# Performance work log

Hardware: AMD Instinct MI355X
Metric: run time of the kernel (lower is better)

Reference implementation:

```python
import jax, jax.numpy as jnp
import numpy as np

B, S, HID, NH = 4, 8192, 1024, 32
DH = HID // NH  # 32 == NH, required by the module's broadcast multiply


def setup_inputs() -> dict:
    key = jax.random.key(0)
    ks = jax.random.split(key, 9)
    scale = 1.0 / np.sqrt(HID)
    return {
        "query": jax.random.normal(ks[0], (B, S, HID), jnp.float32),
        "key": jax.random.normal(ks[1], (B, S, HID), jnp.float32),
        "value": jax.random.normal(ks[2], (B, S, HID), jnp.float32),
        "Wq": jax.random.normal(ks[3], (HID, HID), jnp.float32) * scale,
        "bq": jnp.zeros((HID,), jnp.float32),
        "Wk": jax.random.normal(ks[4], (HID, HID), jnp.float32) * scale,
        "bk": jnp.zeros((HID,), jnp.float32),
        "Wv": jax.random.normal(ks[5], (HID, HID), jnp.float32) * scale,
        "bv": jnp.zeros((HID,), jnp.float32),
    }


def reference(query, key, value, Wq, bq, Wk, bk, Wv, bv):
    # Linear projections (torch Linear: x @ W.T + b)
    q = (query @ Wq.T + bq).reshape(B, S, NH, DH)
    k = (key @ Wk.T + bk).reshape(B, S, NH, DH)
    v = (value @ Wv.T + bv).reshape(B, S, NH, DH)
    # NOTE: source does NOT transpose heads to a batch dim, so matmul
    # contracts head_dim per-token: scores[b,s,h,t] over heads h,t.
    scores = jnp.einsum('bshd,bstd->bsht', q, k) / jnp.sqrt(jnp.float32(HID))
    scores = jax.nn.softmax(scores, axis=-1)  # softmax over heads axis t
    # Dropout is identity in inference mode.
    # Elementwise broadcast multiply [B,S,H,H] * [B,S,H,DH] (H == DH)
    out = scores * v
    return out.reshape(B, S, HID)
```

## Files before the change

kernel.cpp:

```cpp
#include <hip/hip_runtime.h>
#include <hip/hip_bf16.h>


typedef __attribute__((ext_vector_type(8))) short bf16x8;
typedef __attribute__((ext_vector_type(4))) float f32x4;

#define HID 1024

#define GLOAD_LDS16(gp, lp)                                                   \
  __builtin_amdgcn_global_load_lds(                                           \
      (const __attribute__((address_space(1))) void*)(gp),                    \
      (__attribute__((address_space(3))) void*)(lp), 16, 0, 0)

#define SBAR __builtin_amdgcn_sched_barrier(0)

__device__ __forceinline__ unsigned short f2bf(float f) {
  unsigned int u = __builtin_bit_cast(unsigned int, f);
  u += 0x7FFFu + ((u >> 16) & 1u);
  return (unsigned short)(u >> 16);
}
__device__ __forceinline__ float bf2f(unsigned short h) {
  unsigned int u = (unsigned int)h << 16;
  return __builtin_bit_cast(float, u);
}

__device__ __forceinline__ uint2 cvt4(f32x4 a) {
  uint2 r;
  asm("v_cvt_pk_bf16_f32 %0, %1, %2" : "=v"(r.x) : "v"(a[0]), "v"(a[1]));
  asm("v_cvt_pk_bf16_f32 %0, %1, %2" : "=v"(r.y) : "v"(a[2]), "v"(a[3]));
  return r;
}
__device__ __forceinline__ bf16x8 cvt8(f32x4 a, f32x4 b) {
  union { unsigned int u[4]; bf16x8 v; } r;
  asm("v_cvt_pk_bf16_f32 %0, %1, %2" : "=v"(r.u[0]) : "v"(a[0]), "v"(a[1]));
  asm("v_cvt_pk_bf16_f32 %0, %1, %2" : "=v"(r.u[1]) : "v"(a[2]), "v"(a[3]));
  asm("v_cvt_pk_bf16_f32 %0, %1, %2" : "=v"(r.u[2]) : "v"(b[0]), "v"(b[1]));
  asm("v_cvt_pk_bf16_f32 %0, %1, %2" : "=v"(r.u[3]) : "v"(b[2]), "v"(b[3]));
  return r.v;
}

__global__ __launch_bounds__(256)
void convw_kernel(const float* __restrict__ src, unsigned short* __restrict__ dst) {
  const int i = blockIdx.x * 256 + threadIdx.x;
  const f32x4 a = ((const f32x4*)src)[i * 2];
  const f32x4 b = ((const f32x4*)src)[i * 2 + 1];
  ((bf16x8*)dst)[i] = cvt8(a, b);
}

template<int MODE>
__global__ __launch_bounds__(512, 1)
void gemm256(const float* __restrict__ X, const unsigned short* __restrict__ Wb,
             const float* __restrict__ bias, void* outp,
             const unsigned short* __restrict__ pbf) {
  const int bid = blockIdx.x;
  const int L = (bid & 7) * 64 + (bid >> 3);
  const int m0 = (L >> 2) * 256;
  const int n0 = (L & 3) * 256;
  const int tid = threadIdx.x;
  const int lane = tid & 63;
  const int wid = tid >> 6;
  const int wm = (wid >> 2) * 128;
  const int wn = (wid & 3) * 64;
  const int lo = lane & 15, grp = lane >> 4;

  __shared__ __align__(16) unsigned char lds[2][65536];

  const char* Xc = (const char*)X;
  const int acg = tid & 15;
  size_t asrc[8]; int aldst[8];
#pragma unroll
  for (int i = 0; i < 8; ++i) {
    const int row = i * 32 + (tid >> 4);
    asrc[i] = (size_t)(m0 + row) * 4096 + (size_t)(acg * 16);
    aldst[i] = row * 128 + (((acg >> 1) ^ (row & 7)) << 4) + (acg & 1) * 8;
  }
  f32x4 ar[8];
  auto aload = [&](int kt) {
    const size_t kb = (size_t)kt * 256;
#pragma unroll
    for (int i = 0; i < 8; ++i) ar[i] = *(const f32x4*)(Xc + asrc[i] + kb);
  };
  auto awrite = [&](int b) {
#pragma unroll
    for (int i = 0; i < 8; ++i) *(uint2*)&lds[b][aldst[i]] = cvt4(ar[i]);
  };

  const char* Wc = (const char*)Wb;
  size_t bsrc[4];
#pragma unroll
  for (int i = 0; i < 4; ++i) {
    const int g = tid + i * 512;
    const int row = g >> 3, j = g & 7;
    bsrc[i] = (size_t)(n0 + row) * 2048 + (size_t)((j ^ (row & 7)) << 4);
  }
  auto bstage = [&](int b, int kt) {
    const size_t kb = (size_t)kt * 128;
#pragma unroll
    for (int i = 0; i < 4; ++i)
      GLOAD_LDS16(Wc + bsrc[i] + kb, &lds[b][32768 + tid * 16 + i * 8192]);
  };

  f32x4 acc[8][4] = {};
  auto compute = [&](int b) {
#pragma unroll
    for (int kk = 0; kk < 2; ++kk) {
      const int s = kk * 4 + grp;
      bf16x8 af[8], bfm[4];
#pragma unroll
      for (int f = 0; f < 8; ++f) {
        const int ra = wm + f * 16 + lo;
        af[f] = *(const bf16x8*)&lds[b][ra * 128 + ((s ^ (ra & 7)) << 4)];
      }
#pragma unroll
      for (int g = 0; g < 4; ++g) {
        const int rb = wn + g * 16 + lo;
        bfm[g] = *(const bf16x8*)&lds[b][32768 + rb * 128 + ((s ^ (rb & 7)) << 4)];
      }
      __builtin_amdgcn_s_setprio(1);
#pragma unroll
      for (int fm = 0; fm < 8; ++fm)
#pragma unroll
        for (int fn = 0; fn < 4; ++fn)
          acc[fm][fn] = __builtin_amdgcn_mfma_f32_16x16x32_bf16(
              af[fm], bfm[fn], acc[fm][fn], 0, 0, 0);
      __builtin_amdgcn_s_setprio(0);
    }
  };

  aload(0);
  awrite(0);
  SBAR;
  bstage(0, 0);
  SBAR;
  aload(1);
  SBAR;
  asm volatile("s_waitcnt vmcnt(8)" ::: "memory");
  asm volatile("s_waitcnt lgkmcnt(0)" ::: "memory");
  __builtin_amdgcn_s_barrier();
  SBAR;

#pragma unroll 1
  for (int kt = 0; kt < 16; ++kt) {
    const int cur = kt & 1;
    if (kt < 15) {
      awrite(cur ^ 1);
      SBAR;
      bstage(cur ^ 1, kt + 1);
      SBAR;
      if (kt < 14) aload(kt + 2);
      SBAR;
    }
    compute(cur);
    SBAR;
    if (kt < 14) asm volatile("s_waitcnt vmcnt(8)" ::: "memory");
    else         asm volatile("s_waitcnt vmcnt(0)" ::: "memory");
    asm volatile("s_waitcnt lgkmcnt(0)" ::: "memory");
    __builtin_amdgcn_s_barrier();
    SBAR;
  }

  if (MODE == 2) {
    float* of = (float*)outp;
#pragma unroll
    for (int fm = 0; fm < 8; ++fm) {
      const int row = m0 + wm + fm * 16 + grp * 4;
#pragma unroll
      for (int fn = 0; fn < 4; ++fn) {
        const int col = n0 + wn + fn * 16 + lo;
        const float bc = bias[col];
#pragma unroll
        for (int j = 0; j < 4; ++j) {
          const size_t idx = (size_t)(row + j) * 1024 + col;
          of[idx] = bf2f(pbf[idx]) * (acc[fm][fn][j] + bc);
        }
      }
    }
  } else {
    const float scale = (MODE == 0) ? 0.03125f : 1.0f;
    unsigned short* lds16 = (unsigned short*)&lds[0][0];
    unsigned short* ob = (unsigned short*)outp;
    const int half = (MODE == 1) ? 1024 : 0;
    float bcol[4];
#pragma unroll
    for (int fn = 0; fn < 4; ++fn) bcol[fn] = bias[n0 + wn + fn * 16 + lo];
#pragma unroll 1
    for (int h = 0; h < 2; ++h) {
      if ((wid >> 2) == h) {
#pragma unroll
        for (int fm = 0; fm < 8; ++fm)
#pragma unroll
          for (int fn = 0; fn < 4; ++fn)
#pragma unroll
            for (int j = 0; j < 4; ++j) {
              const int rl = fm * 16 + grp * 4 + j;
              const int col = wn + fn * 16 + lo;
              lds16[rl * 256 + (col ^ (grp << 4))] =
                  f2bf((acc[fm][fn][j] + bcol[fn]) * scale);
            }
      }
      __syncthreads();
      {
        const int row = tid >> 2;
        const int c0 = (tid & 3) * 64;
        const int x = ((row >> 2) & 3) << 4;
#pragma unroll
        for (int q = 0; q < 8; ++q) {
          const int cg = c0 + q * 8;
          const uint4 v = *(const uint4*)&lds16[row * 256 + (cg ^ x)];
          *(uint4*)&ob[(size_t)(m0 + h * 128 + row) * 2048 + half + n0 + cg] = v;
        }
      }
      __syncthreads();
    }
  }
}

template<int MODE>
__global__ __launch_bounds__(256, 2)
void gemm_fb(const float* __restrict__ X, const float* __restrict__ W,
             const float* __restrict__ bias, void* outp,
             const unsigned short* __restrict__ pbf, int use_ws) {
  const int bid = blockIdx.x;
  const int L = (bid & 7) * 256 + (bid >> 3);
  const int m0 = (L >> 3) * 128;
  const int n0 = (L & 7) * 128;
  const int tid = threadIdx.x;
  const int lane = tid & 63;
  const int wid = tid >> 6;
  const int wm = (wid >> 1) << 6;
  const int wn = (wid & 1) << 6;
  const int lo = lane & 15, grp = lane >> 4;
  __shared__ __align__(16) unsigned char lds[2][32768];
  const int srow = tid >> 3;
  const int sk8  = tid & 7;
  const float* Ag = X + (size_t)(m0 + srow) * HID + sk8 * 8;
  const float* Bg = W + (size_t)(n0 + srow) * HID + sk8 * 8;
  f32x4 la[4][2], lb[4][2];
  auto gload = [&](int k0) {
#pragma unroll
    for (int rr = 0; rr < 4; ++rr) {
      const float* ap = Ag + (size_t)(rr * 32) * HID + k0;
      const float* bp = Bg + (size_t)(rr * 32) * HID + k0;
      la[rr][0] = *(const f32x4*)(ap); la[rr][1] = *(const f32x4*)(ap + 4);
      lb[rr][0] = *(const f32x4*)(bp); lb[rr][1] = *(const f32x4*)(bp + 4);
    }
  };
  auto cvtwrite = [&](int b) {
#pragma unroll
    for (int rr = 0; rr < 4; ++rr) {
      const int row = srow + rr * 32;
      const int adr = row * 128 + ((sk8 ^ (row & 7)) << 4);
      *(bf16x8*)&lds[b][adr]         = cvt8(la[rr][0], la[rr][1]);
      *(bf16x8*)&lds[b][16384 + adr] = cvt8(lb[rr][0], lb[rr][1]);
    }
  };
  f32x4 acc[4][4] = {};
  auto compute = [&](int b) {
#pragma unroll
    for (int kk = 0; kk < 2; ++kk) {
      const int slot = kk * 4 + grp;
      bf16x8 af[4], bfm[4];
#pragma unroll
      for (int f = 0; f < 4; ++f) {
        const int ra = wm + f * 16 + lo;
        const int rb = wn + f * 16 + lo;
        af[f]  = *(const bf16x8*)&lds[b][ra * 128 + ((slot ^ (ra & 7)) << 4)];
        bfm[f] = *(const bf16x8*)&lds[b][16384 + rb * 128 + ((slot ^ (rb & 7)) << 4)];
      }
#pragma unroll
      for (int fm = 0; fm < 4; ++fm)
#pragma unroll
        for (int fn = 0; fn < 4; ++fn)
          acc[fm][fn] = __builtin_amdgcn_mfma_f32_16x16x32_bf16(
              af[fm], bfm[fn], acc[fm][fn], 0, 0, 0);
    }
  };
  gload(0); cvtwrite(0); gload(64);
  SBAR;
  asm volatile("s_waitcnt lgkmcnt(0)" ::: "memory");
  __builtin_amdgcn_s_barrier();
  SBAR;
#pragma unroll 1
  for (int kt = 0; kt < 16; ++kt) {
    compute(kt & 1);
    if (kt < 15) {
      cvtwrite((kt + 1) & 1);
      if (kt < 14) gload((kt + 2) * 64);
    }
    SBAR;
    asm volatile("s_waitcnt lgkmcnt(0)" ::: "memory");
    __builtin_amdgcn_s_barrier();
    SBAR;
  }
  unsigned char* eb = &lds[0][0];
  const unsigned char* ebc = eb;
  if (MODE == 2) {
    float* of = (float*)outp;
#pragma unroll
    for (int fm = 0; fm < 4; ++fm) {
      const int row = m0 + wm + fm * 16 + grp * 4;
#pragma unroll
      for (int fn = 0; fn < 4; ++fn) {
        const int col = n0 + wn + fn * 16 + lo;
        const float bc = bias[col];
#pragma unroll
        for (int j = 0; j < 4; ++j) {
          const size_t idx = (size_t)(row + j) * 1024 + col;
          const float p = use_ws ? bf2f(pbf[idx]) : of[idx];
          of[idx] = p * (acc[fm][fn][j] + bc);
        }
      }
    }
  } else {
    const float scale = (MODE == 0) ? 0.03125f : 1.0f;
#pragma unroll
    for (int fm = 0; fm < 4; ++fm) {
#pragma unroll
      for (int fn = 0; fn < 4; ++fn) {
        const int colL = wn + fn * 16 + lo;
        const float bc = bias[n0 + colL];
#pragma unroll
        for (int j = 0; j < 4; ++j) {
          const int rowL = wm + fm * 16 + grp * 4 + j;
          const int byte = rowL * 256 + ((colL * 2) ^ ((rowL & 7) << 5));
          *(unsigned short*)&eb[byte] = f2bf((acc[fm][fn][j] + bc) * scale);
        }
      }
    }
    __syncthreads();
    unsigned short* ob = (unsigned short*)outp;
    const int half = (MODE == 1) ? 1024 : 0;
#pragma unroll
    for (int p = 0; p < 8; ++p) {
      const int r = p * 16 + (tid >> 4);
      const int c0 = (tid & 15) * 8;
      const uint4 v = *(const uint4*)&ebc[r * 256 + ((c0 * 2) ^ ((r & 7) << 5))];
      *(uint4*)&ob[(size_t)(m0 + r) * 2048 + half + n0 + c0] = v;
    }
  }
}

template<int PMODE>
__global__ __launch_bounds__(256)
void attn_kernel(float* __restrict__ dout, unsigned short* __restrict__ wsp) {
  const int wid = threadIdx.x >> 6;
  const int lane = threadIdx.x & 63;
  const int token = blockIdx.x * 4 + wid;
  const int lo = lane & 15, grp = lane >> 4;
  const unsigned short* qk = (const unsigned short*)dout + (size_t)token * 2048;
  const int base = lo * 32 + grp * 8;

  bf16x8 a0 = *(const bf16x8*)(qk + base);
  bf16x8 a1 = *(const bf16x8*)(qk + 512 + base);
  bf16x8 b0 = *(const bf16x8*)(qk + 1024 + base);
  bf16x8 b1 = *(const bf16x8*)(qk + 1536 + base);
  asm volatile("s_waitcnt vmcnt(0)" ::: "memory");

  const f32x4 z = {0.f, 0.f, 0.f, 0.f};
  f32x4 s[2][2];
  s[0][0] = __builtin_amdgcn_mfma_f32_16x16x32_bf16(a0, b0, z, 0, 0, 0);
  s[0][1] = __builtin_amdgcn_mfma_f32_16x16x32_bf16(a0, b1, z, 0, 0, 0);
  s[1][0] = __builtin_amdgcn_mfma_f32_16x16x32_bf16(a1, b0, z, 0, 0, 0);
  s[1][1] = __builtin_amdgcn_mfma_f32_16x16x32_bf16(a1, b1, z, 0, 0, 0);

  float* od = dout + (size_t)token * 1024;
  unsigned short* ob = wsp + (size_t)token * 1024;
#pragma unroll
  for (int rt = 0; rt < 2; ++rt) {
#pragma unroll
    for (int j = 0; j < 4; ++j) {
      const float v0 = s[rt][0][j], v1 = s[rt][1][j];
      float m = fmaxf(v0, v1);
#pragma unroll
      for (int msk = 1; msk < 16; msk <<= 1) m = fmaxf(m, __shfl_xor(m, msk, 64));
      const float e0 = __expf(v0 - m), e1 = __expf(v1 - m);
      float ssum = e0 + e1;
#pragma unroll
      for (int msk = 1; msk < 16; msk <<= 1) ssum += __shfl_xor(ssum, msk, 64);
      const float inv = 1.0f / ssum;
      const int h = rt * 16 + grp * 4 + j;
      if (PMODE == 0) {
        od[h * 32 + lo]      = e0 * inv;
        od[h * 32 + 16 + lo] = e1 * inv;
      } else {
        ob[h * 32 + lo]      = f2bf(e0 * inv);
        ob[h * 32 + 16 + lo] = f2bf(e1 * inv);
      }
    }
  }
}

extern "C" void kernel_launch(void* const* d_in, const int* in_sizes, int n_in,
                              void* d_out, int out_size, void* d_ws, size_t ws_size,
                              hipStream_t stream) {
  const float* query = (const float*)d_in[0];
  const float* key   = (const float*)d_in[1];
  const float* value = (const float*)d_in[2];
  const float* Wq    = (const float*)d_in[3];
  const float* bq    = (const float*)d_in[4];
  const float* Wk    = (const float*)d_in[5];
  const float* bk    = (const float*)d_in[6];
  const float* Wv    = (const float*)d_in[7];
  const float* bv    = (const float*)d_in[8];

  const size_t P_BYTES = (size_t)32768 * 1024 * 2;
  const size_t W_BYTES = (size_t)1024 * 1024 * 2;
  unsigned short* pbf = (unsigned short*)d_ws;
  unsigned short* Wqb = (unsigned short*)((char*)d_ws + P_BYTES);
  unsigned short* Wkb = Wqb + (W_BYTES / 2);
  unsigned short* Wvb = Wkb + (W_BYTES / 2);

  if (ws_size >= P_BYTES + 3 * W_BYTES) {
    convw_kernel<<<dim3(512), dim3(256), 0, stream>>>(Wq, Wqb);
    convw_kernel<<<dim3(512), dim3(256), 0, stream>>>(Wk, Wkb);
    convw_kernel<<<dim3(512), dim3(256), 0, stream>>>(Wv, Wvb);
    gemm256<0><<<dim3(512), dim3(512), 0, stream>>>(query, Wqb, bq, d_out, pbf);
    gemm256<1><<<dim3(512), dim3(512), 0, stream>>>(key,   Wkb, bk, d_out, pbf);
    attn_kernel<1><<<dim3(8192), dim3(256), 0, stream>>>((float*)d_out, pbf);
    gemm256<2><<<dim3(512), dim3(512), 0, stream>>>(value, Wvb, bv, d_out, pbf);
  } else {
    const int use_ws = (ws_size >= P_BYTES) ? 1 : 0;
    gemm_fb<0><<<dim3(2048), dim3(256), 0, stream>>>(query, Wq, bq, d_out, nullptr, 0);
    gemm_fb<1><<<dim3(2048), dim3(256), 0, stream>>>(key,   Wk, bk, d_out, nullptr, 0);
    if (use_ws)
      attn_kernel<1><<<dim3(8192), dim3(256), 0, stream>>>((float*)d_out, pbf);
    else
      attn_kernel<0><<<dim3(8192), dim3(256), 0, stream>>>((float*)d_out, nullptr);
    gemm_fb<2><<<dim3(2048), dim3(256), 0, stream>>>(value, Wv, bv, d_out, pbf, use_ws);
  }
}
```

Before: 378.1 us.

## Interleave LDS reads, global prefetch and MFMA in four barrier-synced phases

The GEMM main loop changes from a monolithic stage-then-compute body to four phases per k-tile. Each phase loads part of the A/B fragments from LDS, issues part of the next tile's global-to-LDS staging, then runs a quarter of the MFMAs between workgroup barriers. The goal is to overlap memory traffic with matrix-core work, in the style of ping-pong scheduling, and to cut register pressure by holding only half the A fragments at once. In exchange the loop has more barriers and waits per iteration.

Measured after the change: 412.0 us. 9.0% more time.

```diff
diff --git a/kernel.cpp b/kernel.cpp
--- a/kernel.cpp
+++ b/kernel.cpp
@@ -93,44 +93,57 @@
     const int row = g >> 3, j = g & 7;
     bsrc[i] = (size_t)(n0 + row) * 2048 + (size_t)((j ^ (row & 7)) << 4);
   }
-  auto bstage = [&](int b, int kt) {
+  auto bstage_h = [&](int b, int kt, int h) {
     const size_t kb = (size_t)kt * 128;
 #pragma unroll
-    for (int i = 0; i < 4; ++i)
+    for (int i = 2 * h; i < 2 * h + 2; ++i)
       GLOAD_LDS16(Wc + bsrc[i] + kb, &lds[b][32768 + tid * 16 + i * 8192]);
   };
 
   f32x4 acc[8][4] = {};
-  auto compute = [&](int b) {
-#pragma unroll
-    for (int kk = 0; kk < 2; ++kk) {
-      const int s = kk * 4 + grp;
-      bf16x8 af[8], bfm[4];
-#pragma unroll
-      for (int f = 0; f < 8; ++f) {
-        const int ra = wm + f * 16 + lo;
-        af[f] = *(const bf16x8*)&lds[b][ra * 128 + ((s ^ (ra & 7)) << 4)];
-      }
-#pragma unroll
-      for (int g = 0; g < 4; ++g) {
-        const int rb = wn + g * 16 + lo;
-        bfm[g] = *(const bf16x8*)&lds[b][32768 + rb * 128 + ((s ^ (rb & 7)) << 4)];
-      }
-      __builtin_amdgcn_s_setprio(1);
-#pragma unroll
-      for (int fm = 0; fm < 8; ++fm)
-#pragma unroll
-        for (int fn = 0; fn < 4; ++fn)
-          acc[fm][fn] = __builtin_amdgcn_mfma_f32_16x16x32_bf16(
-              af[fm], bfm[fn], acc[fm][fn], 0, 0, 0);
-      __builtin_amdgcn_s_setprio(0);
-    }
-  };
+  bf16x8 af[4], bfr[4];
+  auto rdB = [&](int b, int kk) {
+#pragma unroll
+    for (int g = 0; g < 4; ++g) {
+      const int rb = wn + g * 16 + lo;
+      bfr[g] = *(const bf16x8*)&lds[b][32768 + rb * 128 +
+                                       (((kk * 4 + grp) ^ (rb & 7)) << 4)];
+    }
+  };
+  auto rdA = [&](int b, int kk, int fh) {
+#pragma unroll
+    for (int f = 0; f < 4; ++f) {
+      const int ra = wm + (fh * 4 + f) * 16 + lo;
+      af[f] = *(const bf16x8*)&lds[b][ra * 128 +
+                                      (((kk * 4 + grp) ^ (ra & 7)) << 4)];
+    }
+  };
+  auto mfma4 = [&](int fh) {
+    __builtin_amdgcn_s_setprio(1);
+#pragma unroll
+    for (int f = 0; f < 4; ++f)
+#pragma unroll
+      for (int g = 0; g < 4; ++g)
+        acc[fh * 4 + f][g] = __builtin_amdgcn_mfma_f32_16x16x32_bf16(
+            af[f], bfr[g], acc[fh * 4 + f][g], 0, 0, 0);
+    __builtin_amdgcn_s_setprio(0);
+  };
+
+#define PHASE_SYNC                                                 \
+  SBAR;                                                            \
+  __builtin_amdgcn_s_barrier();                                    \
+  asm volatile("s_waitcnt lgkmcnt(0)" ::: "memory");               \
+  SBAR;
+#define PHASE_END                                                  \
+  SBAR;                                                            \
+  __builtin_amdgcn_s_barrier();                                    \
+  SBAR;
 
   aload(0);
   awrite(0);
   SBAR;
-  bstage(0, 0);
+  bstage_h(0, 0, 0);
+  bstage_h(0, 0, 1);
   SBAR;
   aload(1);
   SBAR;
@@ -141,20 +154,31 @@
 
 #pragma unroll 1
   for (int kt = 0; kt < 16; ++kt) {
-    const int cur = kt & 1;
-    if (kt < 15) {
-      awrite(cur ^ 1);
-      SBAR;
-      bstage(cur ^ 1, kt + 1);
-      SBAR;
-      if (kt < 14) aload(kt + 2);
-      SBAR;
-    }
-    compute(cur);
+    const int cur = kt & 1, nxt = cur ^ 1;
+    rdB(cur, 0);
+    rdA(cur, 0, 0);
+    if (kt < 15) bstage_h(nxt, kt + 1, 0);
+    PHASE_SYNC;
+    mfma4(0);
+    PHASE_END;
+    rdA(cur, 0, 1);
+    if (kt < 15) bstage_h(nxt, kt + 1, 1);
+    PHASE_SYNC;
+    mfma4(1);
+    PHASE_END;
+    rdB(cur, 1);
+    rdA(cur, 1, 0);
+    if (kt < 15) awrite(nxt);
+    PHASE_SYNC;
+    mfma4(0);
+    PHASE_END;
+    rdA(cur, 1, 1);
+    if (kt < 14) aload(kt + 2);
+    PHASE_SYNC;
+    mfma4(1);
     SBAR;
     if (kt < 14) asm volatile("s_waitcnt vmcnt(8)" ::: "memory");
     else         asm volatile("s_waitcnt vmcnt(0)" ::: "memory");
-    asm volatile("s_waitcnt lgkmcnt(0)" ::: "memory");
     __builtin_amdgcn_s_barrier();
     SBAR;
   }
```

## Deepen GEMM pipeline: triple-buffer B tiles and double A register prefetch

Applied to the files above, without the earlier changes.

Restructures the GEMM main loop so the weight (B) tiles are triple-buffered in LDS and staged two k-steps ahead, while the activation (A) tiles use two register sets loaded three k-steps ahead. The aim is to hide more global-memory latency behind the MFMA compute. In exchange it uses more LDS (160KB per block), more VGPRs for the second register set, and more complex vmcnt accounting that could be fragile.

Result: slower. 780.5 us (+106.4%).

```diff
diff --git a/kernel.cpp b/kernel.cpp
--- a/kernel.cpp
+++ b/kernel.cpp
@@ -63,7 +63,7 @@
   const int wn = (wid & 3) * 64;
   const int lo = lane & 15, grp = lane >> 4;
 
-  __shared__ __align__(16) unsigned char lds[2][65536];
+  __shared__ __align__(16) unsigned char lds[163840];
 
   const char* Xc = (const char*)X;
   const int acg = tid & 15;
@@ -74,15 +74,24 @@
     asrc[i] = (size_t)(m0 + row) * 4096 + (size_t)(acg * 16);
     aldst[i] = row * 128 + (((acg >> 1) ^ (row & 7)) << 4) + (acg & 1) * 8;
   }
-  f32x4 ar[8];
-  auto aload = [&](int kt) {
+  f32x4 ar0[8], ar1[8];
+  auto aload0 = [&](int kt) {
     const size_t kb = (size_t)kt * 256;
 #pragma unroll
-    for (int i = 0; i < 8; ++i) ar[i] = *(const f32x4*)(Xc + asrc[i] + kb);
-  };
-  auto awrite = [&](int b) {
-#pragma unroll
-    for (int i = 0; i < 8; ++i) *(uint2*)&lds[b][aldst[i]] = cvt4(ar[i]);
+    for (int i = 0; i < 8; ++i) ar0[i] = *(const f32x4*)(Xc + asrc[i] + kb);
+  };
+  auto aload1 = [&](int kt) {
+    const size_t kb = (size_t)kt * 256;
+#pragma unroll
+    for (int i = 0; i < 8; ++i) ar1[i] = *(const f32x4*)(Xc + asrc[i] + kb);
+  };
+  auto awrite0 = [&]() {
+#pragma unroll
+    for (int i = 0; i < 8; ++i) *(uint2*)&lds[aldst[i]] = cvt4(ar0[i]);
+  };
+  auto awrite1 = [&]() {
+#pragma unroll
+    for (int i = 0; i < 8; ++i) *(uint2*)&lds[32768 + aldst[i]] = cvt4(ar1[i]);
   };
 
   const char* Wc = (const char*)Wb;
@@ -95,13 +104,16 @@
   }
   auto bstage = [&](int b, int kt) {
     const size_t kb = (size_t)kt * 128;
+    const int base = 65536 + b * 32768;
 #pragma unroll
     for (int i = 0; i < 4; ++i)
-      GLOAD_LDS16(Wc + bsrc[i] + kb, &lds[b][32768 + tid * 16 + i * 8192]);
+      GLOAD_LDS16(Wc + bsrc[i] + kb, &lds[base + tid * 16 + i * 8192]);
   };
 
   f32x4 acc[8][4] = {};
-  auto compute = [&](int b) {
+  auto compute = [&](int ab, int bb) {
+    const unsigned char* Ab = &lds[ab * 32768];
+    const unsigned char* Bb = &lds[65536 + bb * 32768];
 #pragma unroll
     for (int kk = 0; kk < 2; ++kk) {
       const int s = kk * 4 + grp;
@@ -109,12 +121,12 @@
 #pragma unroll
       for (int f = 0; f < 8; ++f) {
         const int ra = wm + f * 16 + lo;
-        af[f] = *(const bf16x8*)&lds[b][ra * 128 + ((s ^ (ra & 7)) << 4)];
+        af[f] = *(const bf16x8*)&Ab[ra * 128 + ((s ^ (ra & 7)) << 4)];
       }
 #pragma unroll
       for (int g = 0; g < 4; ++g) {
         const int rb = wn + g * 16 + lo;
-        bfm[g] = *(const bf16x8*)&lds[b][32768 + rb * 128 + ((s ^ (rb & 7)) << 4)];
+        bfm[g] = *(const bf16x8*)&Bb[rb * 128 + ((s ^ (rb & 7)) << 4)];
       }
       __builtin_amdgcn_s_setprio(1);
 #pragma unroll
@@ -127,36 +139,46 @@
     }
   };
 
-  aload(0);
-  awrite(0);
+  aload0(0);
+  awrite0();
   SBAR;
   bstage(0, 0);
-  SBAR;
-  aload(1);
-  SBAR;
-  asm volatile("s_waitcnt vmcnt(8)" ::: "memory");
+  bstage(1, 1);
+  SBAR;
+  aload1(1);
+  aload0(2);
+  SBAR;
+  asm volatile("s_waitcnt vmcnt(20)" ::: "memory");
   asm volatile("s_waitcnt lgkmcnt(0)" ::: "memory");
   __builtin_amdgcn_s_barrier();
   SBAR;
 
+  int bb = 0;
 #pragma unroll 1
   for (int kt = 0; kt < 16; ++kt) {
-    const int cur = kt & 1;
+    const int ab = kt & 1;
     if (kt < 15) {
-      awrite(cur ^ 1);
+      if ((kt + 1) & 1) awrite1(); else awrite0();
       SBAR;
-      bstage(cur ^ 1, kt + 1);
+    }
+    if (kt < 14) {
+      int b2 = bb + 2; if (b2 >= 3) b2 -= 3;
+      bstage(b2, kt + 2);
       SBAR;
-      if (kt < 14) aload(kt + 2);
+    }
+    if (kt < 13) {
+      if ((kt + 3) & 1) aload1(kt + 3); else aload0(kt + 3);
       SBAR;
     }
-    compute(cur);
+    compute(ab, bb);
     SBAR;
-    if (kt < 14) asm volatile("s_waitcnt vmcnt(8)" ::: "memory");
-    else         asm volatile("s_waitcnt vmcnt(0)" ::: "memory");
+    if (kt < 13)       asm volatile("s_waitcnt vmcnt(20)" ::: "memory");
+    else if (kt == 13) asm volatile("s_waitcnt vmcnt(12)" ::: "memory");
+    else if (kt == 14) asm volatile("s_waitcnt vmcnt(0)" ::: "memory");
     asm volatile("s_waitcnt lgkmcnt(0)" ::: "memory");
     __builtin_amdgcn_s_barrier();
     SBAR;
+    ++bb; if (bb >= 3) bb = 0;
   }
 
   if (MODE == 2) {
@@ -177,7 +199,7 @@
     }
   } else {
     const float scale = (MODE == 0) ? 0.03125f : 1.0f;
-    unsigned short* lds16 = (unsigned short*)&lds[0][0];
+    unsigned short* lds16 = (unsigned short*)&lds[0];
     unsigned short* ob = (unsigned short*)outp;
     const int half = (MODE == 1) ? 1024 : 0;
     float bcol[4];
```
